# Kernel optimization log

Measured on AMD Instinct MI355X. Metric: run time of the kernel, lower is better.

## Reference

```python
import jax, jax.numpy as jnp
import numpy as np

D_HEAD = 64

def setup_inputs() -> dict:
    key = jax.random.key(0)
    kq, kk, kv, kc = jax.random.split(key, 4)
    B, H, T, D = 2, 16, 2048, D_HEAD
    Q = jax.random.normal(kq, (B, H, T, D), dtype=jnp.float32)
    K = jax.random.normal(kk, (B, H, T, D), dtype=jnp.float32)
    V = jax.random.normal(kv, (B, H, T, D), dtype=jnp.float32)
    # causal mask: True = attend
    mask = jnp.tril(jnp.ones((T, T), dtype=jnp.bool_))
    curvature = jax.random.normal(kc, (H, D, D), dtype=jnp.float32) * 0.02
    return {"Q": Q, "K": K, "V": V, "mask": mask, "curvature": curvature}

def reference(Q, K, V, mask, curvature):
    scale = 1.0 / np.sqrt(Q.shape[-1]).astype(np.float32)
    # per-head learned rotation of Q
    Q_rot = jnp.einsum('bhtd,hde->bhte', Q, curvature)
    scores = jnp.einsum('bhtd,bhsd->bhts', Q_rot, K) * scale  # [B,H,T,T]
    scores = jnp.where(mask[None, None, :, :], scores, -jnp.inf)
    attn = jax.nn.softmax(scores, axis=-1)
    out = jnp.einsum('bhts,bhsd->bhtd', attn, V)
    return out
```

## Files before the change

### kernel.cpp

```cpp
#include <hip/hip_runtime.h>


typedef __attribute__((ext_vector_type(8))) short short8;
typedef __attribute__((ext_vector_type(8))) unsigned short ushort8;
typedef __attribute__((ext_vector_type(4))) float f32x4;
typedef __attribute__((ext_vector_type(4))) _Float16 half4;
typedef __attribute__((ext_vector_type(8))) _Float16 half8;

constexpr int Tc = 2048;
constexpr int Dc = 64;
constexpr size_t REGION = (size_t)32 * Tc * Dc;

__device__ inline unsigned short f2bf(float f) {
    union { float f; unsigned u; } x; x.f = f;
    return (unsigned short)((x.u + 0x7fffu + ((x.u >> 16) & 1u)) >> 16);
}

#define MFMA_BF16_K32(a, b, c) __builtin_amdgcn_mfma_f32_16x16x32_bf16((a), (b), (c), 0, 0, 0)
#define MFMA_F16_K16(a, b, c)  __builtin_amdgcn_mfma_f32_16x16x16f16((a), (b), (c), 0, 0, 0)

__global__ __launch_bounds__(256, 1)
void holo_cfrag(const float* __restrict__ Cp, unsigned short* __restrict__ cfrag_g)
{
    const int t = threadIdx.x, lane = t & 63, eb = t >> 6;
    const int l15 = lane & 15, quad = lane >> 4;
    const int h = blockIdx.x;
    const float* Cg = Cp + (size_t)h * Dc * Dc;
    #pragma unroll
    for (int half = 0; half < 2; ++half) {
        short8 b;
        #pragma unroll
        for (int jj = 0; jj < 8; ++jj) {
            const int d = half * 32 + quad * 8 + jj;
            b[jj] = (short)f2bf(Cg[d * Dc + eb * 16 + l15]);
        }
        *(short8*)(&cfrag_g[(((size_t)h * 4 + eb) * 2 + half) * 512 + lane * 8]) = b;
    }
}

__global__ __launch_bounds__(256, 4)
void holo_prep7(const float* __restrict__ Qp, const float* __restrict__ Kp,
                const float* __restrict__ Vp,
                const unsigned short* __restrict__ cfrag_g,
                unsigned short* __restrict__ qfrag_g,
                unsigned short* __restrict__ kfrag_g,
                _Float16* __restrict__ vfrag_g)
{
    __shared__ unsigned short pf[64 * 72];

    const int t = threadIdx.x, lane = t & 63, w = t >> 6;
    const int l15 = lane & 15, quad = lane >> 4, wb = w * 16;
    const int n = blockIdx.x, bh = n >> 5, st = n & 31, h = bh & 15;
    const int s0 = st * 64;

    {
        const float* Krow = Kp + ((size_t)bh * Tc + s0 + w * 16 + l15) * Dc;
        float4 k0 = *(const float4*)(Krow + quad * 8);
        float4 k1 = *(const float4*)(Krow + quad * 8 + 4);
        float4 k2 = *(const float4*)(Krow + 32 + quad * 8);
        float4 k3 = *(const float4*)(Krow + 32 + quad * 8 + 4);
        ushort8 p0, p1;
        p0[0]=f2bf(k0.x); p0[1]=f2bf(k0.y); p0[2]=f2bf(k0.z); p0[3]=f2bf(k0.w);
        p0[4]=f2bf(k1.x); p0[5]=f2bf(k1.y); p0[6]=f2bf(k1.z); p0[7]=f2bf(k1.w);
        p1[0]=f2bf(k2.x); p1[1]=f2bf(k2.y); p1[2]=f2bf(k2.z); p1[3]=f2bf(k2.w);
        p1[4]=f2bf(k3.x); p1[5]=f2bf(k3.y); p1[6]=f2bf(k3.z); p1[7]=f2bf(k3.w);
        unsigned short* kdst = kfrag_g + (((size_t)(bh * 32 + st) * 4 + w) * 64 + lane) * 16;
        *(ushort8*)(kdst) = p0;
        *(ushort8*)(kdst + 8) = p1;
    }

    {
        const float* Vt = Vp + ((size_t)bh * Tc + s0) * Dc;
        half8 v0, v1;
        #pragma unroll
        for (int dn = 0; dn < 2; ++dn)
            #pragma unroll
            for (int i = 0; i < 4; ++i)
                v0[dn * 4 + i] = (_Float16)Vt[(w * 16 + quad * 4 + i) * Dc + dn * 16 + l15];
        #pragma unroll
        for (int dn = 0; dn < 2; ++dn)
            #pragma unroll
            for (int i = 0; i < 4; ++i)
                v1[dn * 4 + i] = (_Float16)Vt[(w * 16 + quad * 4 + i) * Dc + (dn + 2) * 16 + l15];
        _Float16* vdst = vfrag_g + (((size_t)(bh * 32 + st) * 4 + w) * 64 + lane) * 16;
        *(half8*)(vdst) = v0;
        *(half8*)(vdst + 8) = v1;
    }

    {
        const float* Qrow = Qp + ((size_t)bh * Tc + s0 + wb + l15) * Dc;
        float4 q0v = *(const float4*)(Qrow + quad * 8);
        float4 q1v = *(const float4*)(Qrow + quad * 8 + 4);
        float4 q2v = *(const float4*)(Qrow + 32 + quad * 8);
        float4 q3v = *(const float4*)(Qrow + 32 + quad * 8 + 4);
        short8 a0, a1;
        a0[0]=(short)f2bf(q0v.x); a0[1]=(short)f2bf(q0v.y); a0[2]=(short)f2bf(q0v.z); a0[3]=(short)f2bf(q0v.w);
        a0[4]=(short)f2bf(q1v.x); a0[5]=(short)f2bf(q1v.y); a0[6]=(short)f2bf(q1v.z); a0[7]=(short)f2bf(q1v.w);
        a1[0]=(short)f2bf(q2v.x); a1[1]=(short)f2bf(q2v.y); a1[2]=(short)f2bf(q2v.z); a1[3]=(short)f2bf(q2v.w);
        a1[4]=(short)f2bf(q3v.x); a1[5]=(short)f2bf(q3v.y); a1[6]=(short)f2bf(q3v.z); a1[7]=(short)f2bf(q3v.w);
        #pragma unroll
        for (int eb = 0; eb < 4; ++eb) {
            short8 b0 = *(const short8*)(&cfrag_g[(((size_t)h * 4 + eb) * 2 + 0) * 512 + lane * 8]);
            short8 b1 = *(const short8*)(&cfrag_g[(((size_t)h * 4 + eb) * 2 + 1) * 512 + lane * 8]);
            f32x4 c = {0.f, 0.f, 0.f, 0.f};
            c = MFMA_BF16_K32(a0, b0, c);
            c = MFMA_BF16_K32(a1, b1, c);
            #pragma unroll
            for (int i = 0; i < 4; ++i)
                pf[(wb + quad * 4 + i) * 72 + eb * 16 + l15] = f2bf(c[i] * 0.18033688f);
        }
        __threadfence_block();
        short8 fa0 = *(const short8*)(&pf[(wb + l15) * 72 + quad * 8]);
        short8 fa1 = *(const short8*)(&pf[(wb + l15) * 72 + 32 + quad * 8]);
        const size_t strip = (size_t)bh * 128 + st * 4 + w;
        *(short8*)(&qfrag_g[strip * 1024 + lane * 8]) = fa0;
        *(short8*)(&qfrag_g[strip * 1024 + 512 + lane * 8]) = fa1;
    }
}

__global__ __launch_bounds__(256, 4)
void holo_attn7(const unsigned short* __restrict__ qfrag_g,
                const unsigned short* __restrict__ kfrag_g,
                const _Float16* __restrict__ vfrag_g,
                float* __restrict__ Op)
{
    const int t = threadIdx.x, lane = t & 63, wid = t >> 6;
    const int l15 = lane & 15, quad = lane >> 4, wb = wid * 16;

    const int id = blockIdx.x;
    const int xcd = id & 7, m = (id >> 3) & 31, k = id >> 8;
    const int bh = xcd * 4 + k;
    const int mm = (k >= 2) ? ((m + 16) & 31) : m;
    const int qi = (k & 1) ? (31 - mm) : mm;
    const int q0 = qi * 64;

    short8 qa0, qa1;
    {
        const size_t strip = (size_t)bh * 128 + qi * 4 + wid;
        qa0 = *(const short8*)(&qfrag_g[strip * 1024 + lane * 8]);
        qa1 = *(const short8*)(&qfrag_g[strip * 1024 + 512 + lane * 8]);
    }

    const unsigned short* kbase = kfrag_g + (size_t)bh * 32 * 4 * 1024;
    const _Float16*       vbase = vfrag_g + (size_t)bh * 32 * 4 * 1024;

    f32x4 o[4];
    float l_lane = 0.f;
    #pragma unroll
    for (int dn = 0; dn < 4; ++dn) o[dn] = f32x4{0.f, 0.f, 0.f, 0.f};

    const int rowg = q0 + wb + l15;

    short8 kf0[4], kf1[4];
    #pragma unroll
    for (int tn = 0; tn < 4; ++tn) {
        const unsigned short* kfb = kbase + ((size_t)tn * 64 + lane) * 16;
        kf0[tn] = *(const short8*)(kfb);
        kf1[tn] = *(const short8*)(kfb + 8);
    }

    for (int j = 0; j <= qi; ++j) {
        half8 vlo[4], vhi[4];
        #pragma unroll
        for (int tn = 0; tn < 4; ++tn) {
            const _Float16* vfb = vbase + (size_t)j * 4096 + ((size_t)tn * 64 + lane) * 16;
            vlo[tn] = *(const half8*)(vfb);
            vhi[tn] = *(const half8*)(vfb + 8);
        }

        f32x4 st[4];
        #pragma unroll
        for (int tn = 0; tn < 4; ++tn) {
            f32x4 c = {0.f, 0.f, 0.f, 0.f};
            c = MFMA_BF16_K32(kf0[tn], qa0, c);
            c = MFMA_BF16_K32(kf1[tn], qa1, c);
            st[tn] = c;
        }

        {
            const int jn = (j < qi) ? j + 1 : j;
            #pragma unroll
            for (int tn = 0; tn < 4; ++tn) {
                const unsigned short* kfb = kbase + (size_t)jn * 4096 + ((size_t)tn * 64 + lane) * 16;
                kf0[tn] = *(const short8*)(kfb);
                kf1[tn] = *(const short8*)(kfb + 8);
            }
        }

        half4 pa[4];
        #pragma unroll
        for (int tn = 0; tn < 4; ++tn) {
            #pragma unroll
            for (int i = 0; i < 4; ++i) {
                float sv = st[tn][i];
                if (j == qi) {
                    const int colg = j * 64 + tn * 16 + quad * 4 + i;
                    if (colg > rowg) sv = -1e30f;
                }
                const float p = __builtin_amdgcn_exp2f(sv);
                l_lane += p;
                pa[tn][i] = (_Float16)p;
            }
        }

        #pragma unroll
        for (int tn = 0; tn < 4; ++tn) {
            half4 vf0 = __builtin_shufflevector(vlo[tn], vlo[tn], 0, 1, 2, 3);
            half4 vf1 = __builtin_shufflevector(vlo[tn], vlo[tn], 4, 5, 6, 7);
            half4 vf2 = __builtin_shufflevector(vhi[tn], vhi[tn], 0, 1, 2, 3);
            half4 vf3 = __builtin_shufflevector(vhi[tn], vhi[tn], 4, 5, 6, 7);
            o[0] = MFMA_F16_K16(vf0, pa[tn], o[0]);
            o[1] = MFMA_F16_K16(vf1, pa[tn], o[1]);
            o[2] = MFMA_F16_K16(vf2, pa[tn], o[2]);
            o[3] = MFMA_F16_K16(vf3, pa[tn], o[3]);
        }
    }

    l_lane += __shfl_xor(l_lane, 16);
    l_lane += __shfl_xor(l_lane, 32);
    const float inv = 1.0f / l_lane;

    float* dst = Op + ((size_t)bh * Tc + rowg) * Dc;
    #pragma unroll
    for (int dn = 0; dn < 4; ++dn) {
        float4 r;
        r.x = o[dn][0] * inv; r.y = o[dn][1] * inv;
        r.z = o[dn][2] * inv; r.w = o[dn][3] * inv;
        *(float4*)(&dst[dn * 16 + quad * 4]) = r;
    }
}

extern "C" void kernel_launch(void* const* d_in, const int* in_sizes, int n_in,
                              void* d_out, int out_size, void* d_ws, size_t ws_size,
                              hipStream_t stream) {
    const float* Q = (const float*)d_in[0];
    const float* K = (const float*)d_in[1];
    const float* V = (const float*)d_in[2];
    const float* C = (const float*)d_in[4];
    float* O = (float*)d_out;

    unsigned short* qfrag_w = (unsigned short*)d_ws;
    unsigned short* kfrag_w = qfrag_w + REGION;
    _Float16*       vfrag_w = (_Float16*)(kfrag_w + REGION);
    unsigned short* cfrag_w = (unsigned short*)(vfrag_w + REGION);

    holo_cfrag<<<dim3(16), dim3(256), 0, stream>>>(C, cfrag_w);
    holo_prep7<<<dim3(1024), dim3(256), 0, stream>>>(Q, K, V, cfrag_w, qfrag_w, kfrag_w, vfrag_w);
    holo_attn7<<<dim3(1024), dim3(256), 0, stream>>>(qfrag_w, kfrag_w, vfrag_w, O);
}
```

Before: 160.2 us.

## Stage prep loads through LDS, prefetch V one tile ahead, pack P conversion

The prep kernel now loads Q, K and V tiles with fully coalesced float4 reads into padded LDS buffers. It converts them there and builds the fragments from LDS, replacing the old strided per-element V gathers. The attention kernel prefetches the next V tile after the PV MFMAs, as it already does for K, and uses the packed round-toward-zero fp16 conversion for the probabilities. This adds LDS footprint and a barrier in prep, and changes rounding of P slightly.

Result: faster. 145.7 us (-9.1%).

```diff
diff --git a/kernel.cpp b/kernel.cpp
--- a/kernel.cpp
+++ b/kernel.cpp
@@ -4,6 +4,7 @@
 typedef __attribute__((ext_vector_type(8))) short short8;
 typedef __attribute__((ext_vector_type(8))) unsigned short ushort8;
 typedef __attribute__((ext_vector_type(4))) float f32x4;
+typedef __attribute__((ext_vector_type(2))) _Float16 half2v;
 typedef __attribute__((ext_vector_type(4))) _Float16 half4;
 typedef __attribute__((ext_vector_type(8))) _Float16 half8;
 
@@ -14,6 +15,10 @@
 __device__ inline unsigned short f2bf(float f) {
     union { float f; unsigned u; } x; x.f = f;
     return (unsigned short)((x.u + 0x7fffu + ((x.u >> 16) & 1u)) >> 16);
+}
+
+__device__ inline half2v pkrtz(float a, float b) {
+    return __builtin_bit_cast(half2v, __builtin_amdgcn_cvt_pkrtz(a, b));
 }
 
 #define MFMA_BF16_K32(a, b, c) __builtin_amdgcn_mfma_f32_16x16x32_bf16((a), (b), (c), 0, 0, 0)
@@ -39,13 +44,16 @@
 }
 
 __global__ __launch_bounds__(256, 4)
-void holo_prep7(const float* __restrict__ Qp, const float* __restrict__ Kp,
+void holo_prep8(const float* __restrict__ Qp, const float* __restrict__ Kp,
                 const float* __restrict__ Vp,
                 const unsigned short* __restrict__ cfrag_g,
                 unsigned short* __restrict__ qfrag_g,
                 unsigned short* __restrict__ kfrag_g,
                 _Float16* __restrict__ vfrag_g)
 {
+    __shared__ unsigned short kt[64 * 72];
+    __shared__ unsigned short qt[64 * 72];
+    __shared__ _Float16      vt[64 * 72];
     __shared__ unsigned short pf[64 * 72];
 
     const int t = threadIdx.x, lane = t & 63, w = t >> 6;
@@ -53,51 +61,57 @@
     const int n = blockIdx.x, bh = n >> 5, st = n & 31, h = bh & 15;
     const int s0 = st * 64;
 
-    {
-        const float* Krow = Kp + ((size_t)bh * Tc + s0 + w * 16 + l15) * Dc;
-        float4 k0 = *(const float4*)(Krow + quad * 8);
-        float4 k1 = *(const float4*)(Krow + quad * 8 + 4);
-        float4 k2 = *(const float4*)(Krow + 32 + quad * 8);
-        float4 k3 = *(const float4*)(Krow + 32 + quad * 8 + 4);
-        ushort8 p0, p1;
-        p0[0]=f2bf(k0.x); p0[1]=f2bf(k0.y); p0[2]=f2bf(k0.z); p0[3]=f2bf(k0.w);
-        p0[4]=f2bf(k1.x); p0[5]=f2bf(k1.y); p0[6]=f2bf(k1.z); p0[7]=f2bf(k1.w);
-        p1[0]=f2bf(k2.x); p1[1]=f2bf(k2.y); p1[2]=f2bf(k2.z); p1[3]=f2bf(k2.w);
-        p1[4]=f2bf(k3.x); p1[5]=f2bf(k3.y); p1[6]=f2bf(k3.z); p1[7]=f2bf(k3.w);
+    const float* Qg = Qp + ((size_t)bh * Tc + s0) * Dc;
+    const float* Kg = Kp + ((size_t)bh * Tc + s0) * Dc;
+    const float* Vg = Vp + ((size_t)bh * Tc + s0) * Dc;
+
+    #pragma unroll
+    for (int kk = 0; kk < 4; ++kk) {
+        const int flat = kk * 1024 + t * 4;
+        const int r = flat >> 6, d0 = flat & 63;
+        float4 kv = *(const float4*)(&Kg[flat]);
+        ushort4 kp; kp.x = f2bf(kv.x); kp.y = f2bf(kv.y); kp.z = f2bf(kv.z); kp.w = f2bf(kv.w);
+        *(ushort4*)(&kt[r * 72 + d0]) = kp;
+        float4 qv = *(const float4*)(&Qg[flat]);
+        ushort4 qp; qp.x = f2bf(qv.x); qp.y = f2bf(qv.y); qp.z = f2bf(qv.z); qp.w = f2bf(qv.w);
+        *(ushort4*)(&qt[r * 72 + d0]) = qp;
+        float4 vv = *(const float4*)(&Vg[flat]);
+        half4 vp;
+        vp[0] = (_Float16)vv.x; vp[1] = (_Float16)vv.y;
+        vp[2] = (_Float16)vv.z; vp[3] = (_Float16)vv.w;
+        *(half4*)(&vt[r * 72 + d0]) = vp;
+    }
+    __syncthreads();
+
+    {
+        const int row = wb + l15;
+        ushort8 p0 = *(const ushort8*)(&kt[row * 72 + quad * 8]);
+        ushort8 p1 = *(const ushort8*)(&kt[row * 72 + 32 + quad * 8]);
         unsigned short* kdst = kfrag_g + (((size_t)(bh * 32 + st) * 4 + w) * 64 + lane) * 16;
         *(ushort8*)(kdst) = p0;
         *(ushort8*)(kdst + 8) = p1;
     }
 
     {
-        const float* Vt = Vp + ((size_t)bh * Tc + s0) * Dc;
         half8 v0, v1;
         #pragma unroll
         for (int dn = 0; dn < 2; ++dn)
             #pragma unroll
             for (int i = 0; i < 4; ++i)
-                v0[dn * 4 + i] = (_Float16)Vt[(w * 16 + quad * 4 + i) * Dc + dn * 16 + l15];
+                v0[dn * 4 + i] = vt[(wb + quad * 4 + i) * 72 + dn * 16 + l15];
         #pragma unroll
         for (int dn = 0; dn < 2; ++dn)
             #pragma unroll
             for (int i = 0; i < 4; ++i)
-                v1[dn * 4 + i] = (_Float16)Vt[(w * 16 + quad * 4 + i) * Dc + (dn + 2) * 16 + l15];
+                v1[dn * 4 + i] = vt[(wb + quad * 4 + i) * 72 + (dn + 2) * 16 + l15];
         _Float16* vdst = vfrag_g + (((size_t)(bh * 32 + st) * 4 + w) * 64 + lane) * 16;
         *(half8*)(vdst) = v0;
         *(half8*)(vdst + 8) = v1;
     }
 
     {
-        const float* Qrow = Qp + ((size_t)bh * Tc + s0 + wb + l15) * Dc;
-        float4 q0v = *(const float4*)(Qrow + quad * 8);
-        float4 q1v = *(const float4*)(Qrow + quad * 8 + 4);
-        float4 q2v = *(const float4*)(Qrow + 32 + quad * 8);
-        float4 q3v = *(const float4*)(Qrow + 32 + quad * 8 + 4);
-        short8 a0, a1;
-        a0[0]=(short)f2bf(q0v.x); a0[1]=(short)f2bf(q0v.y); a0[2]=(short)f2bf(q0v.z); a0[3]=(short)f2bf(q0v.w);
-        a0[4]=(short)f2bf(q1v.x); a0[5]=(short)f2bf(q1v.y); a0[6]=(short)f2bf(q1v.z); a0[7]=(short)f2bf(q1v.w);
-        a1[0]=(short)f2bf(q2v.x); a1[1]=(short)f2bf(q2v.y); a1[2]=(short)f2bf(q2v.z); a1[3]=(short)f2bf(q2v.w);
-        a1[4]=(short)f2bf(q3v.x); a1[5]=(short)f2bf(q3v.y); a1[6]=(short)f2bf(q3v.z); a1[7]=(short)f2bf(q3v.w);
+        short8 a0 = *(const short8*)(&qt[(wb + l15) * 72 + quad * 8]);
+        short8 a1 = *(const short8*)(&qt[(wb + l15) * 72 + 32 + quad * 8]);
         #pragma unroll
         for (int eb = 0; eb < 4; ++eb) {
             short8 b0 = *(const short8*)(&cfrag_g[(((size_t)h * 4 + eb) * 2 + 0) * 512 + lane * 8]);
@@ -119,7 +133,7 @@
 }
 
 __global__ __launch_bounds__(256, 4)
-void holo_attn7(const unsigned short* __restrict__ qfrag_g,
+void holo_attn8(const unsigned short* __restrict__ qfrag_g,
                 const unsigned short* __restrict__ kfrag_g,
                 const _Float16* __restrict__ vfrag_g,
                 float* __restrict__ Op)
@@ -152,22 +166,18 @@
     const int rowg = q0 + wb + l15;
 
     short8 kf0[4], kf1[4];
+    half8 vlo[4], vhi[4];
     #pragma unroll
     for (int tn = 0; tn < 4; ++tn) {
         const unsigned short* kfb = kbase + ((size_t)tn * 64 + lane) * 16;
         kf0[tn] = *(const short8*)(kfb);
         kf1[tn] = *(const short8*)(kfb + 8);
+        const _Float16* vfb = vbase + ((size_t)tn * 64 + lane) * 16;
+        vlo[tn] = *(const half8*)(vfb);
+        vhi[tn] = *(const half8*)(vfb + 8);
     }
 
     for (int j = 0; j <= qi; ++j) {
-        half8 vlo[4], vhi[4];
-        #pragma unroll
-        for (int tn = 0; tn < 4; ++tn) {
-            const _Float16* vfb = vbase + (size_t)j * 4096 + ((size_t)tn * 64 + lane) * 16;
-            vlo[tn] = *(const half8*)(vfb);
-            vhi[tn] = *(const half8*)(vfb + 8);
-        }
-
         f32x4 st[4];
         #pragma unroll
         for (int tn = 0; tn < 4; ++tn) {
@@ -177,19 +187,18 @@
             st[tn] = c;
         }
 
-        {
-            const int jn = (j < qi) ? j + 1 : j;
-            #pragma unroll
-            for (int tn = 0; tn < 4; ++tn) {
-                const unsigned short* kfb = kbase + (size_t)jn * 4096 + ((size_t)tn * 64 + lane) * 16;
-                kf0[tn] = *(const short8*)(kfb);
-                kf1[tn] = *(const short8*)(kfb + 8);
-            }
+        const int jn = (j < qi) ? j + 1 : j;
+        #pragma unroll
+        for (int tn = 0; tn < 4; ++tn) {
+            const unsigned short* kfb = kbase + (size_t)jn * 4096 + ((size_t)tn * 64 + lane) * 16;
+            kf0[tn] = *(const short8*)(kfb);
+            kf1[tn] = *(const short8*)(kfb + 8);
         }
 
         half4 pa[4];
         #pragma unroll
         for (int tn = 0; tn < 4; ++tn) {
+            float p[4];
             #pragma unroll
             for (int i = 0; i < 4; ++i) {
                 float sv = st[tn][i];
@@ -197,10 +206,12 @@
                     const int colg = j * 64 + tn * 16 + quad * 4 + i;
                     if (colg > rowg) sv = -1e30f;
                 }
-                const float p = __builtin_amdgcn_exp2f(sv);
-                l_lane += p;
-                pa[tn][i] = (_Float16)p;
+                p[i] = __builtin_amdgcn_exp2f(sv);
+                l_lane += p[i];
             }
+            half2v lo = pkrtz(p[0], p[1]);
+            half2v hi = pkrtz(p[2], p[3]);
+            pa[tn] = __builtin_shufflevector(lo, hi, 0, 1, 2, 3);
         }
 
         #pragma unroll
@@ -214,6 +225,13 @@
             o[2] = MFMA_F16_K16(vf2, pa[tn], o[2]);
             o[3] = MFMA_F16_K16(vf3, pa[tn], o[3]);
         }
+
+        #pragma unroll
+        for (int tn = 0; tn < 4; ++tn) {
+            const _Float16* vfb = vbase + (size_t)jn * 4096 + ((size_t)tn * 64 + lane) * 16;
+            vlo[tn] = *(const half8*)(vfb);
+            vhi[tn] = *(const half8*)(vfb + 8);
+        }
     }
 
     l_lane += __shfl_xor(l_lane, 16);
@@ -245,6 +263,6 @@
     unsigned short* cfrag_w = (unsigned short*)(vfrag_w + REGION);
 
     holo_cfrag<<<dim3(16), dim3(256), 0, stream>>>(C, cfrag_w);
-    holo_prep7<<<dim3(1024), dim3(256), 0, stream>>>(Q, K, V, cfrag_w, qfrag_w, kfrag_w, vfrag_w);
-    holo_attn7<<<dim3(1024), dim3(256), 0, stream>>>(qfrag_w, kfrag_w, vfrag_w, O);
-}
+    holo_prep8<<<dim3(1024), dim3(256), 0, stream>>>(Q, K, V, cfrag_w, qfrag_w, kfrag_w, vfrag_w);
+    holo_attn8<<<dim3(1024), dim3(256), 0, stream>>>(qfrag_w, kfrag_w, vfrag_w, O);
+}
```
